# Kernel optimization log

Measured on AMD Instinct MI355X. Metric: run time of the kernel, lower is better.

## Reference

```python
import jax, jax.numpy as jnp
import numpy as np

NUM_HEADS = 16
NEG_INF = -1e9


def setup_inputs() -> dict:
    key = jax.random.key(0)
    ks = jax.random.split(key, 12)
    T, B, E = 2048, 4, 1024
    s = 0.02
    inp = {
        "query": jax.random.normal(ks[0], (T, B, E), jnp.float32),
        "key": jax.random.normal(ks[1], (T, B, E), jnp.float32),
        "value": jax.random.normal(ks[2], (T, B, E), jnp.float32),
        # causal additive mask [T, S]: 0 on/below diagonal, -1e9 above
        "attn_mask": jnp.where(
            jnp.arange(T)[:, None] >= jnp.arange(T)[None, :], 0.0, NEG_INF
        ).astype(jnp.float32),
        "wq": jax.random.normal(ks[3], (E, E), jnp.float32) * s,
        "bq": jax.random.normal(ks[4], (E,), jnp.float32) * s,
        "wk": jax.random.normal(ks[5], (E, E), jnp.float32) * s,
        "bk": jax.random.normal(ks[6], (E,), jnp.float32) * s,
        "wv": jax.random.normal(ks[7], (E, E), jnp.float32) * s,
        "bv": jax.random.normal(ks[8], (E,), jnp.float32) * s,
        "wo": jax.random.normal(ks[9], (E, E), jnp.float32) * s,
        "bo": jax.random.normal(ks[10], (E,), jnp.float32) * s,
    }
    return inp


def reference(query, key, value, attn_mask, wq, bq, wk, bk, wv, bv, wo, bo):
    T, B, E = query.shape
    H = NUM_HEADS
    D = E // H
    scaling = D ** (-0.5)
    # projections (torch Linear: x @ W.T + b)
    q = (query @ wq.T + bq) * scaling          # [T, B, E]
    k = key @ wk.T + bk                         # [S, B, E]
    v = value @ wv.T + bv                       # [S, B, E]
    # -> [B*H, len, D]
    q = q.reshape(T, B * H, D).transpose(1, 0, 2)
    k = k.reshape(-1, B * H, D).transpose(1, 0, 2)
    v = v.reshape(-1, B * H, D).transpose(1, 0, 2)
    # scores [B*H, T, S], additive mask, softmax (dropout = identity in eval)
    attn_weights = jnp.einsum('ntd,nsd->nts', q, k) + attn_mask
    attn_weights = jax.nn.softmax(attn_weights, axis=-1)
    attn = jnp.einsum('nts,nsd->ntd', attn_weights, v)   # [B*H, T, D]
    attn = attn.transpose(1, 0, 2).reshape(T, B, E)
    return attn @ wo.T + bo
```

## Files before the change

kernel.cpp:

```cpp
#include <hip/hip_runtime.h>
#include <hip/hip_bf16.h>

typedef __hip_bfloat16 bf16;
typedef __attribute__((ext_vector_type(8))) short short8;
typedef __attribute__((ext_vector_type(4))) float float4v;
typedef __attribute__((ext_vector_type(2))) unsigned long long ull2;
typedef __attribute__((ext_vector_type(2))) unsigned int uint2v;

#define TLEN  2048
#define BATCH 4
#define EMB   1024
#define HEADS 16
#define HD    64
#define MROWS (TLEN*BATCH)
#define PSTRIDE 72
#define SMAX2 5.770780f
#define QSCALE 0.18033688f

#if __has_builtin(__builtin_amdgcn_exp2f)
#define EXP2(x) __builtin_amdgcn_exp2f(x)
#else
#define EXP2(x) exp2f(x)
#endif

__device__ __forceinline__ unsigned cvt_pk_bf16(float lo, float hi) {
    unsigned r;
    asm("v_cvt_pk_bf16_f32 %0, %1, %2" : "=v"(r) : "v"(lo), "v"(hi));
    return r;
}

__device__ __forceinline__ void gl2lds16(const bf16* g, bf16* l) {
    __builtin_amdgcn_global_load_lds(
        (const __attribute__((address_space(1))) void*)g,
        (__attribute__((address_space(3))) void*)l, 16, 0, 0);
}

__device__ __forceinline__ void store_out(float* p, float v)  { *p = v; }
__device__ __forceinline__ void store_out(bf16* p, float v)   { *p = __float2bfloat16(v); }

__device__ __forceinline__ void cvt8(const float* __restrict__ src,
                                     bf16* __restrict__ dst, int t) {
    const float4v a = ((const float4v*)src)[2*t];
    const float4v b = ((const float4v*)src)[2*t + 1];
    union { short8 v; bf16 h[8]; } u;
    u.h[0] = __float2bfloat16(a[0]);
    u.h[1] = __float2bfloat16(a[1]);
    u.h[2] = __float2bfloat16(a[2]);
    u.h[3] = __float2bfloat16(a[3]);
    u.h[4] = __float2bfloat16(b[0]);
    u.h[5] = __float2bfloat16(b[1]);
    u.h[6] = __float2bfloat16(b[2]);
    u.h[7] = __float2bfloat16(b[3]);
    ((short8*)dst)[t] = u.v;
}

__global__ __launch_bounds__(256)
void cvt_all(const float* __restrict__ q, const float* __restrict__ k,
             const float* __restrict__ v,
             const float* __restrict__ wq, const float* __restrict__ wk,
             const float* __restrict__ wv, const float* __restrict__ wo,
             bf16* __restrict__ xq, bf16* __restrict__ xk, bf16* __restrict__ xv,
             bf16* __restrict__ wqb, bf16* __restrict__ wkb,
             bf16* __restrict__ wvb, bf16* __restrict__ wob)
{
    const int id = blockIdx.x * 256 + threadIdx.x;
    const int NA = 1 << 20, NW = 1 << 17;
    if (id < 3*NA) {
        const int w = id >> 20, off = id & (NA - 1);
        const float* s = w == 0 ? q : (w == 1 ? k : v);
        bf16*        d = w == 0 ? xq : (w == 1 ? xk : xv);
        cvt8(s, d, off);
    } else {
        const int id2 = id - 3*NA;
        const int w = id2 >> 17, off = id2 & (NW - 1);
        const float* s = w == 0 ? wq : (w == 1 ? wk : (w == 2 ? wv : wo));
        bf16*        d = w == 0 ? wqb : (w == 1 ? wkb : (w == 2 ? wvb : wob));
        cvt8(s, d, off);
    }
}

template<typename OutT>
__device__ __forceinline__ void gemm_body(
    const bf16* __restrict__ A, const bf16* __restrict__ Bw,
    const float* __restrict__ bias, OutT* __restrict__ out,
    float scale, int mode, int bm, int bn)
{
    __shared__ __align__(16) bf16 smem[128*64*4];
    const int tid  = threadIdx.x;
    const int lane = tid & 63;
    const int wave = tid >> 6;
    const int wm   = (wave >> 1) * 64;
    const int wn   = (wave & 1) * 64;
    const int quad = lane >> 4;
    const int l16  = lane & 15;
    const int hl   = wn >> 6;

    const int srow = tid >> 3;
    const int skc  = (tid & 7) ^ (srow & 7);
    const bf16* Ag = A  + (size_t)(bm*128 + srow)*EMB + skc*8;
    const bf16* Bg = Bw + (size_t)(bn*128 + srow)*EMB + skc*8;

    float4v acc[4][4];
    #pragma unroll
    for (int i=0;i<4;i++)
        #pragma unroll
        for (int j=0;j<4;j++) acc[i][j] = (float4v){0.f,0.f,0.f,0.f};

    #pragma unroll
    for (int g=0; g<4; g++) {
        gl2lds16(Ag + (size_t)g*32*EMB, smem + tid*8 + g*2048);
        gl2lds16(Bg + (size_t)g*32*EMB, smem + 8192 + tid*8 + g*2048);
    }

    for (int t = 0; t < 16; t++) {
        const int cur = (t & 1) << 14;
        __syncthreads();
        if (t + 1 < 16) {
            const int nxt = cur ^ 16384;
            const int k1  = (t + 1) * 64;
            #pragma unroll
            for (int g=0; g<4; g++) {
                gl2lds16(Ag + (size_t)g*32*EMB + k1, smem + nxt + tid*8 + g*2048);
                gl2lds16(Bg + (size_t)g*32*EMB + k1, smem + nxt + 8192 + tid*8 + g*2048);
            }
        }
        const bf16* As = smem + cur;
        const bf16* Bs = smem + cur + 8192;

        #pragma unroll
        for (int half=0; half<2; half++) {
            const int pc = (((half<<2) | quad) ^ (l16 & 7)) * 8;
            short8 af[4], bfr[4];
            #pragma unroll
            for (int i=0;i<4;i++)
                af[i] = *(const short8*)(As + (wm + i*16 + l16)*64 + pc);
            #pragma unroll
            for (int j=0;j<4;j++)
                bfr[j] = *(const short8*)(Bs + (wn + j*16 + l16)*64 + pc);
            #pragma unroll
            for (int i=0;i<4;i++)
                #pragma unroll
                for (int j=0;j<4;j++)
                    acc[i][j] = __builtin_amdgcn_mfma_f32_16x16x32_bf16(
                                    af[i], bfr[j], acc[i][j], 0, 0, 0);
        }
    }

    if (mode != 2) {
        #pragma unroll
        for (int i=0;i<4;i++) {
            #pragma unroll
            for (int j=0;j<4;j++) {
                const int n = bn*128 + wn + j*16 + l16;
                const float bf = bias[n];
                #pragma unroll
                for (int r=0;r<4;r++) {
                    const int m = bm*128 + wm + i*16 + quad*4 + r;
                    const float v = (acc[i][j][r] + bf) * scale;
                    size_t idx;
                    if (mode == 0) {
                        idx = (size_t)m*EMB + n;
                    } else {
                        const int t = m >> 2, b = m & 3;
                        const int h = n >> 6, d = n & 63;
                        idx = (((size_t)(b*HEADS + h))*TLEN + t)*HD + d;
                    }
                    store_out(out + idx, v);
                }
            }
        }
    } else {
        __syncthreads();
        bf16* Tb = smem;
        #pragma unroll
        for (int i=0;i<4;i++) {
            const int tc = (wm >> 4) + i;
            #pragma unroll
            for (int j=0;j<4;j++) {
                const int d = j*16 + l16;
                const float bf = bias[bn*128 + wn + d];
                #pragma unroll
                for (int r=0;r<4;r++) {
                    const float v = acc[i][j][r] + bf;
                    Tb[((((r<<1)|hl)*64 + d) << 5) + ((tc ^ (d & 7)) << 2) + quad]
                        = __float2bfloat16(v);
                }
            }
        }
        __syncthreads();
        bf16* ob = (bf16*)out;
        #pragma unroll
        for (int pass=0; pass<8; pass++) {
            const int row = pass*64 + (tid >> 2);
            const int c16 = tid & 3;
            const int b2  = row >> 7;
            const int h2l = (row >> 6) & 1;
            const int d   = row & 63;
            const int e   = d & 7;
            const unsigned long long lo =
                *(const unsigned long long*)(Tb + (row << 5) + ((( (2*c16)   ^ e) << 2)));
            const unsigned long long hi =
                *(const unsigned long long*)(Tb + (row << 5) + ((( (2*c16+1) ^ e) << 2)));
            ull2 val; val.x = lo; val.y = hi;
            *(ull2*)(ob + ((size_t)((b2*HEADS + bn*2 + h2l)*HD + d))*TLEN
                        + bm*32 + c16*8) = val;
        }
    }
}

__global__ __launch_bounds__(256, 2)
void gemm_qkv(const bf16* __restrict__ xq, const bf16* __restrict__ xk,
              const bf16* __restrict__ xv,
              const bf16* __restrict__ wq, const bf16* __restrict__ wk,
              const bf16* __restrict__ wv,
              const float* __restrict__ bq, const float* __restrict__ bk,
              const float* __restrict__ bv,
              bf16* __restrict__ oq, bf16* __restrict__ ok,
              bf16* __restrict__ ov)
{
    const int id  = blockIdx.x;
    const int xcd = id & 7;
    const int r   = id >> 3;
    const int z   = r >> 6;
    const int rem = r & 63;
    const int bm  = xcd + 8*(rem >> 3);
    const int bn  = rem & 7;

    const bf16*  A  = z == 0 ? xq : (z == 1 ? xk : xv);
    const bf16*  W  = z == 0 ? wq : (z == 1 ? wk : wv);
    const float* bi = z == 0 ? bq : (z == 1 ? bk : bv);
    bf16*        o  = z == 0 ? oq : (z == 1 ? ok : ov);
    const float  sc = z == 0 ? QSCALE : 1.0f;
    const int    md = z == 2 ? 2 : 1;
    gemm_body<bf16>(A, W, bi, o, sc, md, bm, bn);
}

__global__ __launch_bounds__(256, 2)
void gemm_out(const bf16* __restrict__ A, const bf16* __restrict__ W,
              const float* __restrict__ bias, float* __restrict__ out)
{
    const int id  = blockIdx.x;
    const int xcd = id & 7;
    const int r   = id >> 3;
    const int bm  = xcd + 8*(r >> 3);
    const int bn  = r & 7;
    gemm_body<float>(A, W, bias, out, 1.0f, 0, bm, bn);
}

__global__ __launch_bounds__(256, 2)
void flash_attn(const bf16* __restrict__ Q, const bf16* __restrict__ K,
                const bf16* __restrict__ Vt, bf16* __restrict__ Aout)
{
    __shared__ __align__(16) bf16 Ks[2][64*64];
    __shared__ __align__(16) bf16 Vs[2][64*64];
    __shared__ __align__(16) bf16 Ps[4*32*PSTRIDE];
    const int tid  = threadIdx.x;
    const int lane = tid & 63;
    const int wave = tid >> 6;
    const int quad = lane >> 4;
    const int l16  = lane & 15;

    const int id  = blockIdx.x;
    const int xcd = id & 7;
    const int jj  = id >> 3;
    const int bh  = xcd + 8*(jj & 7);
    const int tq  = 15 - (jj >> 3);
    const int qbase = tq*128 + wave*32;

    short8 qf[2][2];
    #pragma unroll
    for (int f=0; f<2; f++) {
        const bf16* qrow = Q + ((size_t)bh*TLEN + qbase + f*16 + l16)*HD;
        qf[f][0] = *(const short8*)(qrow + quad*8);
        qf[f][1] = *(const short8*)(qrow + 32 + quad*8);
    }

    union { short8 v; short h[8]; } onesu;
    #pragma unroll
    for (int z=0; z<8; z++) onesu.h[z] = (short)0x3F80;
    const short8 ones8 = onesu.v;

    float4v o[2][4];
    float4v lsacc[2];
    #pragma unroll
    for (int f=0; f<2; f++) {
        lsacc[f] = (float4v){0.f,0.f,0.f,0.f};
        #pragma unroll
        for (int j=0;j<4;j++) { o[f][j] = (float4v){0.f,0.f,0.f,0.f}; }
    }

    bf16* Pw = Ps + wave*32*PSTRIDE;

    const int srow   = tid >> 3;
    const int schunk = (tid & 7) ^ (srow & 7);
    const bf16* Kg = K  + (size_t)bh*TLEN*HD + (size_t)srow*HD   + schunk*8;
    const bf16* Vg = Vt + (size_t)bh*HD*TLEN + (size_t)srow*TLEN + schunk*8;
    const int ldst = tid*8;

    const int nt = 2*tq + 2;
    gl2lds16(Kg,           &Ks[0][ldst]);
    gl2lds16(Kg + 32*HD,   &Ks[0][32*64 + ldst]);
    gl2lds16(Vg,           &Vs[0][ldst]);
    gl2lds16(Vg + 32*TLEN, &Vs[0][32*64 + ldst]);

    for (int i = 0; i < nt; i++) {
        const int buf = i & 1;
        __syncthreads();
        if (i + 1 < nt) {
            const int nb = buf ^ 1;
            const size_t s0n = (size_t)(i+1)*64;
            gl2lds16(Kg + s0n*HD,        &Ks[nb][ldst]);
            gl2lds16(Kg + (s0n+32)*HD,   &Ks[nb][32*64 + ldst]);
            gl2lds16(Vg + s0n,           &Vs[nb][ldst]);
            gl2lds16(Vg + 32*TLEN + s0n, &Vs[nb][32*64 + ldst]);
        }

        const bool live = (i*64) <= (qbase + 31);
        if (live) {

        float4v scr[2][4];
        #pragma unroll
        for (int f=0; f<2; f++)
            #pragma unroll
            for (int j=0;j<4;j++)
                scr[f][j] = (float4v){-SMAX2,-SMAX2,-SMAX2,-SMAX2};
        __builtin_amdgcn_s_setprio(1);
        #pragma unroll
        for (int h2=0; h2<2; h2++) {
            const int psw = ((h2<<2) | quad) ^ (l16 & 7);
            #pragma unroll
            for (int j=0;j<4;j++) {
                short8 kf = *(const short8*)(&Ks[buf][(j*16 + l16)*64 + psw*8]);
                scr[0][j] = __builtin_amdgcn_mfma_f32_16x16x32_bf16(kf, qf[0][h2], scr[0][j], 0,0,0);
                scr[1][j] = __builtin_amdgcn_mfma_f32_16x16x32_bf16(kf, qf[1][h2], scr[1][j], 0,0,0);
            }
        }
        __builtin_amdgcn_s_setprio(0);

        #pragma unroll
        for (int f=0; f<2; f++) {
            const int t = qbase + f*16 + l16;
            const bool needmask = (i*64 + 63) > (qbase + f*16);
            #pragma unroll
            for (int j=0;j<4;j++) {
                float p0, p1, p2, p3;
                if (needmask) {
                    const int s = i*64 + j*16 + quad*4;
                    p0 = (s   <= t) ? EXP2(scr[f][j][0]) : 0.f;
                    p1 = (s+1 <= t) ? EXP2(scr[f][j][1]) : 0.f;
                    p2 = (s+2 <= t) ? EXP2(scr[f][j][2]) : 0.f;
                    p3 = (s+3 <= t) ? EXP2(scr[f][j][3]) : 0.f;
                } else {
                    p0 = EXP2(scr[f][j][0]);
                    p1 = EXP2(scr[f][j][1]);
                    p2 = EXP2(scr[f][j][2]);
                    p3 = EXP2(scr[f][j][3]);
                }
                uint2v w;
                w.x = cvt_pk_bf16(p0, p1);
                w.y = cvt_pk_bf16(p2, p3);
                *(uint2v*)(Pw + (f*16 + l16)*PSTRIDE + j*16 + quad*4) = w;
            }
        }

        __builtin_amdgcn_s_setprio(1);
        #pragma unroll
        for (int h2=0; h2<2; h2++) {
            const int psw = ((h2<<2) | quad) ^ (l16 & 7);
            short8 pf0 = *(const short8*)(Pw + (l16)*PSTRIDE      + h2*32 + quad*8);
            short8 pf1 = *(const short8*)(Pw + (16 + l16)*PSTRIDE + h2*32 + quad*8);
            lsacc[0] = __builtin_amdgcn_mfma_f32_16x16x32_bf16(pf0, ones8, lsacc[0], 0,0,0);
            lsacc[1] = __builtin_amdgcn_mfma_f32_16x16x32_bf16(pf1, ones8, lsacc[1], 0,0,0);
            #pragma unroll
            for (int j=0;j<4;j++) {
                short8 vf = *(const short8*)(&Vs[buf][(j*16 + l16)*64 + psw*8]);
                o[0][j] = __builtin_amdgcn_mfma_f32_16x16x32_bf16(pf0, vf, o[0][j], 0,0,0);
                o[1][j] = __builtin_amdgcn_mfma_f32_16x16x32_bf16(pf1, vf, o[1][j], 0,0,0);
            }
        }
        __builtin_amdgcn_s_setprio(0);

        }
    }

    const int b = bh >> 4, h = bh & 15;
    #pragma unroll
    for (int f=0; f<2; f++) {
        float rn[4];
        #pragma unroll
        for (int r=0;r<4;r++)
            rn[r] = 1.0f / lsacc[f][r];
        #pragma unroll
        for (int j=0;j<4;j++)
            #pragma unroll
            for (int r=0;r<4;r++) {
                const int t = qbase + f*16 + quad*4 + r;
                const int d = j*16 + l16;
                Aout[((size_t)t*BATCH + b)*EMB + h*64 + d] =
                    __float2bfloat16(o[f][j][r] * rn[r]);
            }
    }
}

extern "C" void kernel_launch(void* const* d_in, const int* in_sizes, int n_in,
                              void* d_out, int out_size, void* d_ws, size_t ws_size,
                              hipStream_t stream)
{
    const float* query = (const float*)d_in[0];
    const float* key   = (const float*)d_in[1];
    const float* value = (const float*)d_in[2];
    const float* wq = (const float*)d_in[4];
    const float* bq = (const float*)d_in[5];
    const float* wk = (const float*)d_in[6];
    const float* bk = (const float*)d_in[7];
    const float* wv = (const float*)d_in[8];
    const float* bv = (const float*)d_in[9];
    const float* wo = (const float*)d_in[10];
    const float* bo = (const float*)d_in[11];

    const size_t actsz = (size_t)MROWS*EMB;
    const size_t wsz   = (size_t)EMB*EMB;
    bf16* xq    = (bf16*)d_ws;
    bf16* xk    = xq  + actsz;
    bf16* xv    = xk  + actsz;
    bf16* wqb   = xv  + actsz;
    bf16* wkb   = wqb + wsz;
    bf16* wvb   = wkb + wsz;
    bf16* wob   = wvb + wsz;
    bf16* q_ws  = wob + wsz;
    bf16* k_ws  = q_ws + actsz;
    bf16* v_ws  = k_ws + actsz;

    const dim3 blk(256);

    hipLaunchKernelGGL(cvt_all, dim3(14336), blk, 0, stream,
                       query, key, value, wq, wk, wv, wo,
                       xq, xk, xv, wqb, wkb, wvb, wob);

    hipLaunchKernelGGL(gemm_qkv, dim3(1536), blk, 0, stream,
                       xq, xk, xv, wqb, wkb, wvb, bq, bk, bv, q_ws, k_ws, v_ws);

    hipLaunchKernelGGL(flash_attn, dim3(1024), blk, 0, stream, q_ws, k_ws, v_ws, xq);

    hipLaunchKernelGGL(gemm_out, dim3(512), blk, 0, stream, xq, wob, bo, (float*)d_out);
}
```

Measured before the change: 292.5 us.

## Split QKV GEMM into a 256x256-tile Q/K kernel and separate V kernel

Replaces the fused QKV projection GEMM with a new 512-thread kernel that computes Q and K using 256x256 tiles. It double-buffers LDS and uses direct global-to-LDS loads, partial vmcnt waits and setprio around the MFMAs. V stays on the old 128x128 path with its transposed output in a separate launch. Larger tiles raise arithmetic intensity and cut operand reloads, but give only 256 blocks for Q/K, add a launch, and use more registers per thread for accumulators.

After: 301.3 us. 1.03x slower.

```diff
diff --git a/kernel.cpp b/kernel.cpp
--- a/kernel.cpp
+++ b/kernel.cpp
@@ -79,6 +79,115 @@
     }
 }
 
+__global__ __launch_bounds__(512, 2)
+void gemm_qk8(const bf16* __restrict__ xq, const bf16* __restrict__ xk,
+              const bf16* __restrict__ wq, const bf16* __restrict__ wk,
+              const float* __restrict__ bq, const float* __restrict__ bk,
+              bf16* __restrict__ oq, bf16* __restrict__ ok)
+{
+    __shared__ __align__(16) bf16 sm8[2*16384];
+    const int tid  = threadIdx.x;
+    const int lane = tid & 63;
+    const int wave = tid >> 6;
+    const int wm2  = wave >> 2;
+    const int wn2  = wave & 3;
+    const int quad = lane >> 4;
+    const int l16  = lane & 15;
+    const int e3   = l16 & 3;
+
+    const int id = blockIdx.x;
+    const int z  = (id >> 2) & 1;
+    const int bn = id & 3;
+    const int bm = id >> 3;
+
+    const bf16*  A   = z ? xk : xq;
+    const bf16*  W   = z ? wk : wq;
+    const float* bi  = z ? bk : bq;
+    bf16*        out = z ? ok : oq;
+    const float  sc  = z ? 1.0f : QSCALE;
+
+    const int srow = tid >> 2;
+    const int skc  = (tid & 3) ^ (srow & 3);
+    const bf16* Ag = A + (size_t)(bm*256 + srow)*EMB + skc*8;
+    const bf16* Wg = W + (size_t)(bn*256 + srow)*EMB + skc*8;
+
+    float4v acc[8][4];
+    #pragma unroll
+    for (int i=0;i<8;i++)
+        #pragma unroll
+        for (int j=0;j<4;j++) acc[i][j] = (float4v){0.f,0.f,0.f,0.f};
+
+    #pragma unroll
+    for (int g=0; g<2; g++) {
+        gl2lds16(Ag + (size_t)g*128*EMB, sm8 + g*4096 + tid*8);
+        gl2lds16(Wg + (size_t)g*128*EMB, sm8 + 8192 + g*4096 + tid*8);
+    }
+
+    for (int t = 0; t < 32; t++) {
+        const int cur = (t & 1) << 14;
+        if (t + 1 < 32) {
+            const int nxt = cur ^ 16384;
+            const int k1  = (t + 1) * 32;
+            #pragma unroll
+            for (int g=0; g<2; g++) {
+                gl2lds16(Ag + (size_t)g*128*EMB + k1, sm8 + nxt + g*4096 + tid*8);
+                gl2lds16(Wg + (size_t)g*128*EMB + k1, sm8 + nxt + 8192 + g*4096 + tid*8);
+            }
+            asm volatile("s_waitcnt vmcnt(4)" ::: "memory");
+        } else {
+            asm volatile("s_waitcnt vmcnt(0)" ::: "memory");
+        }
+        __builtin_amdgcn_sched_barrier(0);
+        __builtin_amdgcn_s_barrier();
+
+        const bf16* As = sm8 + cur;
+        const bf16* Bs = sm8 + cur + 8192;
+
+        short8 bfr[4];
+        #pragma unroll
+        for (int j=0;j<4;j++) {
+            const int row = wn2*64 + j*16 + l16;
+            bfr[j] = *(const short8*)(Bs + row*32 + (quad ^ e3)*8);
+        }
+
+        #pragma unroll
+        for (int p=0; p<2; p++) {
+            if (p) __builtin_amdgcn_s_barrier();
+            short8 af[4];
+            #pragma unroll
+            for (int i2=0;i2<4;i2++) {
+                const int row = wm2*128 + (p*4 + i2)*16 + l16;
+                af[i2] = *(const short8*)(As + row*32 + (quad ^ e3)*8);
+            }
+            __builtin_amdgcn_s_setprio(1);
+            #pragma unroll
+            for (int i2=0;i2<4;i2++)
+                #pragma unroll
+                for (int j=0;j<4;j++)
+                    acc[p*4+i2][j] = __builtin_amdgcn_mfma_f32_16x16x32_bf16(
+                                         af[i2], bfr[j], acc[p*4+i2][j], 0, 0, 0);
+            __builtin_amdgcn_s_setprio(0);
+        }
+    }
+
+    #pragma unroll
+    for (int i=0;i<8;i++) {
+        #pragma unroll
+        for (int j=0;j<4;j++) {
+            const int n = bn*256 + wn2*64 + j*16 + l16;
+            const float bf = bi[n];
+            const int h = n >> 6, d = n & 63;
+            #pragma unroll
+            for (int r=0;r<4;r++) {
+                const int m = bm*256 + wm2*128 + i*16 + quad*4 + r;
+                const float v = (acc[i][j][r] + bf) * sc;
+                const int tt = m >> 2, b = m & 3;
+                out[(((size_t)(b*HEADS + h))*TLEN + tt)*HD + d] = __float2bfloat16(v);
+            }
+        }
+    }
+}
+
 template<typename OutT>
 __device__ __forceinline__ void gemm_body(
     const bf16* __restrict__ A, const bf16* __restrict__ Bw,
@@ -157,15 +266,7 @@
                 for (int r=0;r<4;r++) {
                     const int m = bm*128 + wm + i*16 + quad*4 + r;
                     const float v = (acc[i][j][r] + bf) * scale;
-                    size_t idx;
-                    if (mode == 0) {
-                        idx = (size_t)m*EMB + n;
-                    } else {
-                        const int t = m >> 2, b = m & 3;
-                        const int h = n >> 6, d = n & 63;
-                        idx = (((size_t)(b*HEADS + h))*TLEN + t)*HD + d;
-                    }
-                    store_out(out + idx, v);
+                    store_out(out + (size_t)m*EMB + n, v);
                 }
             }
         }
@@ -209,30 +310,15 @@
 }
 
 __global__ __launch_bounds__(256, 2)
-void gemm_qkv(const bf16* __restrict__ xq, const bf16* __restrict__ xk,
-              const bf16* __restrict__ xv,
-              const bf16* __restrict__ wq, const bf16* __restrict__ wk,
-              const bf16* __restrict__ wv,
-              const float* __restrict__ bq, const float* __restrict__ bk,
-              const float* __restrict__ bv,
-              bf16* __restrict__ oq, bf16* __restrict__ ok,
-              bf16* __restrict__ ov)
+void gemm_v(const bf16* __restrict__ xv, const bf16* __restrict__ wv,
+            const float* __restrict__ bv, bf16* __restrict__ ov)
 {
     const int id  = blockIdx.x;
     const int xcd = id & 7;
     const int r   = id >> 3;
-    const int z   = r >> 6;
-    const int rem = r & 63;
-    const int bm  = xcd + 8*(rem >> 3);
-    const int bn  = rem & 7;
-
-    const bf16*  A  = z == 0 ? xq : (z == 1 ? xk : xv);
-    const bf16*  W  = z == 0 ? wq : (z == 1 ? wk : wv);
-    const float* bi = z == 0 ? bq : (z == 1 ? bk : bv);
-    bf16*        o  = z == 0 ? oq : (z == 1 ? ok : ov);
-    const float  sc = z == 0 ? QSCALE : 1.0f;
-    const int    md = z == 2 ? 2 : 1;
-    gemm_body<bf16>(A, W, bi, o, sc, md, bm, bn);
+    const int bm  = xcd + 8*(r >> 3);
+    const int bn  = r & 7;
+    gemm_body<bf16>(xv, wv, bv, ov, 1.0f, 2, bm, bn);
 }
 
 __global__ __launch_bounds__(256, 2)
@@ -437,8 +523,10 @@
                        query, key, value, wq, wk, wv, wo,
                        xq, xk, xv, wqb, wkb, wvb, wob);
 
-    hipLaunchKernelGGL(gemm_qkv, dim3(1536), blk, 0, stream,
-                       xq, xk, xv, wqb, wkb, wvb, bq, bk, bv, q_ws, k_ws, v_ws);
+    hipLaunchKernelGGL(gemm_qk8, dim3(256), dim3(512), 0, stream,
+                       xq, xk, wqb, wkb, bq, bk, q_ws, k_ws);
+
+    hipLaunchKernelGGL(gemm_v, dim3(512), blk, 0, stream, xv, wvb, bv, v_ws);
 
     hipLaunchKernelGGL(flash_attn, dim3(1024), blk, 0, stream, q_ws, k_ws, v_ws, xq);
 
```
